# Optimization experiments

Hardware: AMD Instinct MI355X
Metric: run time of the kernel (lower is better)

## Reference

```python
import jax, jax.numpy as jnp
import numpy as np

LORA_ALPHA = 32
RANK = 16
TOP_K = 2
SCALING = LORA_ALPHA / RANK  # lora_alpha / r
EPS = 1e-9


def setup_inputs() -> dict:
    key = jax.random.key(0)
    ks = jax.random.split(key, 6)
    B, S, D_IN, D_OUT, E, R = 4, 2048, 4096, 4096, 8, RANK
    x = jax.random.normal(ks[0], (B, S, D_IN), dtype=jnp.float32)
    W = jax.random.normal(ks[1], (D_OUT, D_IN), dtype=jnp.float32) * (1.0 / np.sqrt(D_IN))
    bias = jax.random.normal(ks[2], (D_OUT,), dtype=jnp.float32) * 0.02
    route_W = jax.random.normal(ks[3], (E, D_IN), dtype=jnp.float32) * (1.0 / np.sqrt(D_IN))
    lora_A = jax.random.normal(ks[4], (E, R, D_IN), dtype=jnp.float32) * (1.0 / np.sqrt(D_IN))
    lora_B = jax.random.normal(ks[5], (D_OUT, R), dtype=jnp.float32)
    lora_B = jnp.broadcast_to(lora_B, (E, D_OUT, R)) * 0.01  # small nonzero so lora path matters
    return {"x": x, "W": W, "bias": bias, "route_W": route_W,
            "lora_A": lora_A, "lora_B": jnp.asarray(lora_B)}


def reference(x, W, bias, route_W, lora_A, lora_B):
    # Base dense projection: y = x W^T + b   [B,S,out]
    base = jnp.einsum('bsi,oi->bso', x, W) + bias

    # Router: softmax over experts in fp32, then top-k gating
    gate_score = jnp.einsum('bsi,ei->bse', x, route_W)          # [B,S,E]
    probs = jax.nn.softmax(gate_score.astype(jnp.float32), axis=-1)
    topk_vals, topk_idx = jax.lax.top_k(probs, TOP_K)           # [B,S,k]
    # renorm (top_k < lora_nums)
    topk_vals = topk_vals / (jnp.sum(topk_vals, axis=-1, keepdims=True) + EPS)
    # dense routing weights: zeros with top-k values scattered back  [B,S,E]
    E = probs.shape[-1]
    routing_weight = jnp.sum(
        jax.nn.one_hot(topk_idx, E, dtype=base.dtype) * topk_vals[..., None].astype(base.dtype),
        axis=-2)

    # Expert LoRA: identical math to the gather/index_add loop, expressed as
    # a dense weighted combine (weights are exactly 0 for unrouted experts).
    xf = x.astype(jnp.float32)
    h = jnp.einsum('bsi,eri->bser', xf, lora_A.astype(jnp.float32))      # [B,S,E,r] (small)
    hw = h * routing_weight.astype(jnp.float32)[..., None]               # gate per expert
    lora_out = jnp.einsum('bser,eor->bso', hw, lora_B.astype(jnp.float32))

    result = base + lora_out.astype(base.dtype) * SCALING
    return result, routing_weight, gate_score
```

## Files before the change

kernel.cpp:

```cpp
#include <hip/hip_runtime.h>
#include <hip/hip_bf16.h>

typedef __bf16 bf16_t;
typedef __bf16 bf16x8 __attribute__((ext_vector_type(8)));
typedef float floatx4 __attribute__((ext_vector_type(4)));

#define M_TOK 8192
#define K_DIM 4096
#define N_OUT 4096
#define NEXP  8
#define LRANK 16
#define KEXT  128
#define SCALING 2.0f

#define GLOAD_LDS16(g, l) \
    __builtin_amdgcn_global_load_lds((const __attribute__((address_space(1))) void*)(g), \
                                     (__attribute__((address_space(3))) void*)(l), 16, 0, 0)


__device__ __forceinline__ void pack4(bf16_t* dst, float4 v) {
    union { bf16_t h[4]; uint2 u; } t;
    t.h[0] = (bf16_t)v.x; t.h[1] = (bf16_t)v.y;
    t.h[2] = (bf16_t)v.z; t.h[3] = (bf16_t)v.w;
    *(uint2*)dst = t.u;
}

__device__ __forceinline__ void cvt8_body(const float* __restrict__ src,
                                          bf16_t* __restrict__ dst, int blk) {
    size_t i = (size_t)blk * 256 + threadIdx.x;
    float4 a = ((const float4*)src)[i * 2];
    float4 b = ((const float4*)src)[i * 2 + 1];
    union { bf16_t h[8]; uint4 u; } t;
    t.h[0] = (bf16_t)a.x; t.h[1] = (bf16_t)a.y; t.h[2] = (bf16_t)a.z; t.h[3] = (bf16_t)a.w;
    t.h[4] = (bf16_t)b.x; t.h[5] = (bf16_t)b.y; t.h[6] = (bf16_t)b.z; t.h[7] = (bf16_t)b.w;
    ((uint4*)dst)[i] = t.u;
}


#define GATE_BLKS     (M_TOK / 16)
#define PREP_W_BLKS   8192
#define PREP_A_BLKS   256
#define PREP_B_BLKS   2048

__global__ __launch_bounds__(256) void prep_gate(const float* __restrict__ x,
                                                 const float* __restrict__ routeW,
                                                 const float* __restrict__ W,
                                                 const float* __restrict__ loraA,
                                                 const float* __restrict__ loraB,
                                                 bf16_t* __restrict__ xb,
                                                 bf16_t* __restrict__ Wb,
                                                 bf16_t* __restrict__ aflat,
                                                 bf16_t* __restrict__ bflat,
                                                 float* __restrict__ rw_out,
                                                 float* __restrict__ gate_out)
{
    __shared__ float rwT[NEXP][256];

    if (blockIdx.x >= GATE_BLKS) {
        int b = blockIdx.x - GATE_BLKS;
        if (b < PREP_W_BLKS) {
            cvt8_body(W, Wb, b);
        } else if (b < PREP_W_BLKS + PREP_A_BLKS) {
            cvt8_body(loraA, aflat, b - PREP_W_BLKS);
        } else {
            int g = (b - PREP_W_BLKS - PREP_A_BLKS) * 256 + threadIdx.x;
            int o = g >> 7, j = g & 127;
            int e = j >> 4, r = j & 15;
            bflat[g] = (bf16_t)loraB[((size_t)e * N_OUT + o) * LRANK + r];
        }
        return;
    }

    int tid = threadIdx.x, lane = tid & 63, wave = tid >> 6;
    int tl = lane >> 4, seg = lane & 15;
    int t = blockIdx.x * 16 + wave * 4 + tl;
    const float* xrow = x + (size_t)t * K_DIM;
    bf16_t* xbrow = xb + (size_t)t * K_DIM;

    float acc[NEXP];
    #pragma unroll
    for (int e = 0; e < NEXP; ++e) acc[e] = 0.f;

    int srow = tid >> 5, scol = (tid & 31) * 8;

    for (int kk = 0; kk < K_DIM / 256; ++kk) {
        {
            const float4* src = (const float4*)(routeW + (size_t)srow * K_DIM + kk * 256 + scol);
            float4 v0 = src[0], v1 = src[1];
            *(float4*)&rwT[srow][scol]     = v0;
            *(float4*)&rwT[srow][scol + 4] = v1;
        }
        __syncthreads();
        #pragma unroll
        for (int kc = 0; kc < 4; ++kc) {
            int kloc = kc * 64 + seg * 4;
            int k = kk * 256 + kloc;
            float4 xv = *(const float4*)(xrow + k);
            union { bf16_t h[4]; uint2 u; } cv;
            cv.h[0] = (bf16_t)xv.x; cv.h[1] = (bf16_t)xv.y;
            cv.h[2] = (bf16_t)xv.z; cv.h[3] = (bf16_t)xv.w;
            *(uint2*)(xbrow + k) = cv.u;
            #pragma unroll
            for (int e = 0; e < NEXP; ++e) {
                float4 wv = *(const float4*)&rwT[e][kloc];
                acc[e] += xv.x * wv.x + xv.y * wv.y + xv.z * wv.z + xv.w * wv.w;
            }
        }
        __syncthreads();
    }

    #pragma unroll
    for (int e = 0; e < NEXP; ++e) {
        acc[e] += __shfl_xor(acc[e], 1);
        acc[e] += __shfl_xor(acc[e], 2);
        acc[e] += __shfl_xor(acc[e], 4);
        acc[e] += __shfl_xor(acc[e], 8);
    }

    if (seg == 0) {
        float mx = acc[0];
        #pragma unroll
        for (int e = 1; e < NEXP; ++e) mx = fmaxf(mx, acc[e]);
        float p[NEXP], s = 0.f;
        #pragma unroll
        for (int e = 0; e < NEXP; ++e) { p[e] = expf(acc[e] - mx); s += p[e]; }
        float inv_s = 1.0f / s;
        #pragma unroll
        for (int e = 0; e < NEXP; ++e) p[e] *= inv_s;
        int i0 = 0;
        #pragma unroll
        for (int e = 1; e < NEXP; ++e) if (p[e] > p[i0]) i0 = e;
        int i1 = (i0 == 0) ? 1 : 0;
        #pragma unroll
        for (int e = 0; e < NEXP; ++e) { if (e == i0 || e == i1) continue; if (p[e] > p[i1]) i1 = e; }
        float v0 = p[i0], v1 = p[i1];
        float inv = 1.0f / (v0 + v1 + 1e-9f);
        float r[NEXP];
        #pragma unroll
        for (int e = 0; e < NEXP; ++e) r[e] = 0.f;
        r[i0] = v0 * inv; r[i1] = v1 * inv;
        #pragma unroll
        for (int e = 0; e < NEXP; ++e) {
            gate_out[(size_t)t * NEXP + e] = acc[e];
            rw_out[(size_t)t * NEXP + e]  = r[e];
        }
    }
}


__global__ __launch_bounds__(256) void h_kernel_v3(const bf16_t* __restrict__ xb,
                                                   const bf16_t* __restrict__ aflat,
                                                   const float* __restrict__ rw,
                                                   bf16_t* __restrict__ hw)
{
    __shared__ bf16_t As[4 * 32 * 32];
    __shared__ bf16_t Bs[4 * 128 * 32];
    int tid = threadIdx.x, lane = tid & 63, wave = tid >> 6;
    int lrow = lane & 15, lq = lane >> 4;
    int n0 = wave * 32;
    int m0 = blockIdx.x * 32;
    floatx4 acc[2][2] = {};

    const bf16_t* srcA[2];
    #pragma unroll
    for (int i = 0; i < 2; ++i) {
        int idx = i * 256 + tid;
        int ks = idx >> 7, r = (idx >> 2) & 31, cc2 = idx & 3;
        srcA[i] = xb + (size_t)(m0 + r) * K_DIM + ks * 32 + cc2 * 8;
    }
    const bf16_t* srcB[8];
    #pragma unroll
    for (int i = 0; i < 8; ++i) {
        int idx = i * 256 + tid;
        int ks = idx >> 9, r = (idx >> 2) & 127, cc2 = idx & 3;
        srcB[i] = aflat + (size_t)r * K_DIM + ks * 32 + cc2 * 8;
    }

    for (int k0 = 0; k0 < K_DIM; k0 += 128) {
        #pragma unroll
        for (int i = 0; i < 2; ++i)
            GLOAD_LDS16(srcA[i] + k0, (char*)As + (i * 256 + wave * 64) * 16);
        #pragma unroll
        for (int i = 0; i < 8; ++i)
            GLOAD_LDS16(srcB[i] + k0, (char*)Bs + (i * 256 + wave * 64) * 16);
        __syncthreads();
        #pragma unroll
        for (int ks = 0; ks < 4; ++ks) {
            bf16x8 af[2], bfr[2];
            #pragma unroll
            for (int mi = 0; mi < 2; ++mi)
                af[mi] = *(const bf16x8*)(As + ks * 1024 + (mi * 16 + lrow) * 32 + lq * 8);
            #pragma unroll
            for (int ni = 0; ni < 2; ++ni)
                bfr[ni] = *(const bf16x8*)(Bs + ks * 4096 + (n0 + ni * 16 + lrow) * 32 + lq * 8);
            #pragma unroll
            for (int mi = 0; mi < 2; ++mi)
                #pragma unroll
                for (int ni = 0; ni < 2; ++ni)
                    acc[mi][ni] = __builtin_amdgcn_mfma_f32_16x16x32_bf16(af[mi], bfr[ni], acc[mi][ni], 0, 0, 0);
        }
        __syncthreads();
    }
    #pragma unroll
    for (int mi = 0; mi < 2; ++mi)
        #pragma unroll
        for (int ni = 0; ni < 2; ++ni)
            #pragma unroll
            for (int reg = 0; reg < 4; ++reg) {
                int t = m0 + mi * 16 + lq * 4 + reg;
                int j = n0 + ni * 16 + lrow;
                float g = rw[(size_t)t * NEXP + (j >> 4)] * SCALING;
                hw[(size_t)t * KEXT + j] = (bf16_t)(acc[mi][ni][reg] * g);
            }
}


#define BM 256
#define BN 256
#define BK 64
#define NT ((K_DIM + KEXT) / BK)

#define STAGE_A(ttv, nxtv, jv) do {                                                         \
    const bf16_t* g_ = ((ttv) < K_DIM / BK)                                                 \
        ? xb + oA + (size_t)(ttv) * BK + (size_t)(jv) * (64 * K_DIM)                        \
        : hw + oEA + (size_t)((ttv) - K_DIM / BK) * BK + (size_t)(jv) * (64 * KEXT);        \
    GLOAD_LDS16(g_, ldA + (nxtv) * (BM * BK * 2) + (jv) * 8192); } while (0)

#define STAGE_B(ttv, nxtv, jv) do {                                                         \
    const bf16_t* g_ = ((ttv) < K_DIM / BK)                                                 \
        ? Wb + oB + (size_t)(ttv) * BK + (size_t)(jv) * (64 * K_DIM)                        \
        : bflat + oEB + (size_t)((ttv) - K_DIM / BK) * BK + (size_t)(jv) * (64 * KEXT);     \
    GLOAD_LDS16(g_, ldB + (nxtv) * (BN * BK * 2) + (jv) * 8192); } while (0)

__global__ __launch_bounds__(512) void main_gemm_v5(const bf16_t* __restrict__ xb,
                                                    const bf16_t* __restrict__ Wb,
                                                    const float* __restrict__ bias,
                                                    const bf16_t* __restrict__ hw,
                                                    const bf16_t* __restrict__ bflat,
                                                    float* __restrict__ out)
{
    __shared__ __align__(16) bf16_t As[2][BM * BK];
    __shared__ __align__(16) bf16_t Bs[2][BN * BK];
    int tid = threadIdx.x, lane = tid & 63, wave = tid >> 6;
    int lrow = lane & 15, lq = lane >> 4;
    int wm = (wave >> 2) * 128;
    int wn = (wave & 3) * 64;

    int lin = blockIdx.y * gridDim.x + blockIdx.x;
    int swzb = (lin & 7) * 64 + (lin >> 3);
    int tm = (swzb >> 4) * BM;
    int tn = (swzb & 15) * BN;

    int swz = lrow & 7;
    int go0 = (lq ^ swz) * 8;
    int go1 = ((4 + lq) ^ swz) * 8;

    int rb = tid >> 3;
    int lg8 = ((tid & 7) ^ (rb & 7)) * 8;
    size_t oA  = (size_t)(tm + rb) * K_DIM + lg8;
    size_t oB  = (size_t)(tn + rb) * K_DIM + lg8;
    size_t oEA = (size_t)(tm + rb) * KEXT + lg8;
    size_t oEB = (size_t)(tn + rb) * KEXT + lg8;
    char* ldA = (char*)As + wave * 1024;
    char* ldB = (char*)Bs + wave * 1024;

    floatx4 acc[8][4] = {};

    #pragma unroll
    for (int j = 0; j < 4; ++j) {
        STAGE_A(0, 0, j);
        STAGE_B(0, 0, j);
    }
    asm volatile("s_waitcnt vmcnt(0)" ::: "memory");
    __builtin_amdgcn_sched_barrier(0);
    __builtin_amdgcn_s_barrier();

    for (int t = 0; t < NT; ++t) {
        int cur = t & 1, nxt = cur ^ 1;
        const bf16_t* curA = &As[cur][(wm + lrow) * BK];
        const bf16_t* curB = &Bs[cur][(wn + lrow) * BK];
        bool pf = (t + 1 < NT);
        int tt = t + 1;

        bf16x8 afA[4][2], afB[4][2], bf0[2][2], bf1[2][2];

        #pragma unroll
        for (int f = 0; f < 4; ++f) {
            afA[f][0] = *(const bf16x8*)(curA + (f * 16) * BK + go0);
            afA[f][1] = *(const bf16x8*)(curA + (f * 16) * BK + go1);
        }
        #pragma unroll
        for (int n = 0; n < 2; ++n) {
            bf0[n][0] = *(const bf16x8*)(curB + (n * 16) * BK + go0);
            bf0[n][1] = *(const bf16x8*)(curB + (n * 16) * BK + go1);
        }
        if (pf) { STAGE_B(tt, nxt, 0); STAGE_B(tt, nxt, 1); }
        __builtin_amdgcn_s_barrier();
        asm volatile("s_waitcnt lgkmcnt(0)" ::: "memory");
        __builtin_amdgcn_sched_barrier(0);
        __builtin_amdgcn_s_setprio(1);
        #pragma unroll
        for (int f = 0; f < 4; ++f)
            #pragma unroll
            for (int n = 0; n < 2; ++n)
                #pragma unroll
                for (int ks = 0; ks < 2; ++ks)
                    acc[f][n] = __builtin_amdgcn_mfma_f32_16x16x32_bf16(afA[f][ks], bf0[n][ks], acc[f][n], 0, 0, 0);
        __builtin_amdgcn_s_setprio(0);
        __builtin_amdgcn_s_barrier();

        #pragma unroll
        for (int n = 0; n < 2; ++n) {
            bf1[n][0] = *(const bf16x8*)(curB + (32 + n * 16) * BK + go0);
            bf1[n][1] = *(const bf16x8*)(curB + (32 + n * 16) * BK + go1);
        }
        if (pf) { STAGE_B(tt, nxt, 2); STAGE_B(tt, nxt, 3); }
        __builtin_amdgcn_s_barrier();
        asm volatile("s_waitcnt lgkmcnt(0)" ::: "memory");
        __builtin_amdgcn_sched_barrier(0);
        __builtin_amdgcn_s_setprio(1);
        #pragma unroll
        for (int f = 0; f < 4; ++f)
            #pragma unroll
            for (int n = 0; n < 2; ++n)
                #pragma unroll
                for (int ks = 0; ks < 2; ++ks)
                    acc[f][2 + n] = __builtin_amdgcn_mfma_f32_16x16x32_bf16(afA[f][ks], bf1[n][ks], acc[f][2 + n], 0, 0, 0);
        __builtin_amdgcn_s_setprio(0);
        if (pf) { asm volatile("s_waitcnt vmcnt(4)" ::: "memory"); }
        else    { asm volatile("s_waitcnt vmcnt(0)" ::: "memory"); }
        __builtin_amdgcn_sched_barrier(0);
        __builtin_amdgcn_s_barrier();

        #pragma unroll
        for (int f = 0; f < 4; ++f) {
            afB[f][0] = *(const bf16x8*)(curA + (64 + f * 16) * BK + go0);
            afB[f][1] = *(const bf16x8*)(curA + (64 + f * 16) * BK + go1);
        }
        if (pf) { STAGE_A(tt, nxt, 0); STAGE_A(tt, nxt, 2); }
        __builtin_amdgcn_s_barrier();
        asm volatile("s_waitcnt lgkmcnt(0)" ::: "memory");
        __builtin_amdgcn_sched_barrier(0);
        __builtin_amdgcn_s_setprio(1);
        #pragma unroll
        for (int f = 0; f < 4; ++f)
            #pragma unroll
            for (int n = 0; n < 2; ++n)
                #pragma unroll
                for (int ks = 0; ks < 2; ++ks)
                    acc[4 + f][n] = __builtin_amdgcn_mfma_f32_16x16x32_bf16(afB[f][ks], bf0[n][ks], acc[4 + f][n], 0, 0, 0);
        __builtin_amdgcn_s_setprio(0);
        __builtin_amdgcn_s_barrier();

        if (pf) { STAGE_A(tt, nxt, 1); STAGE_A(tt, nxt, 3); }
        __builtin_amdgcn_s_barrier();
        __builtin_amdgcn_s_setprio(1);
        #pragma unroll
        for (int f = 0; f < 4; ++f)
            #pragma unroll
            for (int n = 0; n < 2; ++n)
                #pragma unroll
                for (int ks = 0; ks < 2; ++ks)
                    acc[4 + f][2 + n] = __builtin_amdgcn_mfma_f32_16x16x32_bf16(afB[f][ks], bf1[n][ks], acc[4 + f][2 + n], 0, 0, 0);
        __builtin_amdgcn_s_setprio(0);
        if (pf) {
            asm volatile("s_waitcnt vmcnt(2)" ::: "memory");
            __builtin_amdgcn_sched_barrier(0);
        }
        __builtin_amdgcn_s_barrier();
    }

    #pragma unroll
    for (int mh = 0; mh < 2; ++mh)
        #pragma unroll
        for (int f = 0; f < 4; ++f)
            #pragma unroll
            for (int nh = 0; nh < 2; ++nh)
                #pragma unroll
                for (int n = 0; n < 2; ++n) {
                    int row = tm + wm + mh * 64 + f * 16 + lq * 4;
                    int col = tn + wn + nh * 32 + n * 16 + lrow;
                    float b = bias[col];
                    #pragma unroll
                    for (int reg = 0; reg < 4; ++reg)
                        out[(size_t)(row + reg) * N_OUT + col] = acc[mh * 4 + f][nh * 2 + n][reg] + b;
                }
}


__global__ __launch_bounds__(256) void prep_bflat(const float* __restrict__ loraB,
                                                  bf16_t* __restrict__ bflat) {
    int g = blockIdx.x * 256 + threadIdx.x;
    int o = g >> 7, j = g & 127;
    int e = j >> 4, r = j & 15;
    bflat[g] = (bf16_t)loraB[((size_t)e * N_OUT + o) * LRANK + r];
}

__global__ __launch_bounds__(256) void gate_kernel(const float* __restrict__ x,
                                                   const float* __restrict__ routeW,
                                                   float* __restrict__ rw_out,
                                                   float* __restrict__ gate_out)
{
    int wave = threadIdx.x >> 6;
    int lane = threadIdx.x & 63;
    int t = blockIdx.x * 4 + wave;
    const float4* xp = (const float4*)(x + (size_t)t * K_DIM);
    float acc[NEXP];
    #pragma unroll
    for (int e = 0; e < NEXP; ++e) acc[e] = 0.f;
    #pragma unroll 4
    for (int it = 0; it < K_DIM / 256; ++it) {
        float4 xv = xp[it * 64 + lane];
        #pragma unroll
        for (int e = 0; e < NEXP; ++e) {
            float4 wv = ((const float4*)(routeW + (size_t)e * K_DIM))[it * 64 + lane];
            acc[e] += xv.x * wv.x + xv.y * wv.y + xv.z * wv.z + xv.w * wv.w;
        }
    }
    #pragma unroll
    for (int e = 0; e < NEXP; ++e)
        for (int off = 32; off > 0; off >>= 1)
            acc[e] += __shfl_xor(acc[e], off, 64);
    if (lane == 0) {
        float mx = acc[0];
        #pragma unroll
        for (int e = 1; e < NEXP; ++e) mx = fmaxf(mx, acc[e]);
        float p[NEXP], s = 0.f;
        #pragma unroll
        for (int e = 0; e < NEXP; ++e) { p[e] = expf(acc[e] - mx); s += p[e]; }
        float inv_s = 1.0f / s;
        #pragma unroll
        for (int e = 0; e < NEXP; ++e) p[e] *= inv_s;
        int i0 = 0;
        #pragma unroll
        for (int e = 1; e < NEXP; ++e) if (p[e] > p[i0]) i0 = e;
        int i1 = (i0 == 0) ? 1 : 0;
        #pragma unroll
        for (int e = 0; e < NEXP; ++e) { if (e == i0 || e == i1) continue; if (p[e] > p[i1]) i1 = e; }
        float v0 = p[i0], v1 = p[i1];
        float inv = 1.0f / (v0 + v1 + 1e-9f);
        float r[NEXP];
        #pragma unroll
        for (int e = 0; e < NEXP; ++e) r[e] = 0.f;
        r[i0] = v0 * inv; r[i1] = v1 * inv;
        #pragma unroll
        for (int e = 0; e < NEXP; ++e) {
            gate_out[(size_t)t * NEXP + e] = acc[e];
            rw_out[(size_t)t * NEXP + e]  = r[e];
        }
    }
}

__global__ __launch_bounds__(256) void h_kernel(const float* __restrict__ x,
                                                const float* __restrict__ loraA,
                                                const float* __restrict__ rw,
                                                bf16_t* __restrict__ hw)
{
    __shared__ bf16_t As[32][40];
    __shared__ bf16_t Bs[128][40];
    int tid = threadIdx.x;
    int wave = tid >> 6, lane = tid & 63;
    int lrow = lane & 15, lq = lane >> 4;
    int m0 = blockIdx.x * 32;
    floatx4 acc[2][2] = {};
    int rb = tid >> 1, cb = (tid & 1) * 16;
    for (int k0 = 0; k0 < K_DIM; k0 += 32) {
        if (tid < 64) {
            const float* srcA = x + (size_t)(m0 + rb) * K_DIM + k0 + cb;
            #pragma unroll
            for (int q = 0; q < 4; ++q) pack4(&As[rb][cb + q * 4], ((const float4*)srcA)[q]);
        }
        {
            const float* srcB = loraA + (size_t)rb * K_DIM + k0 + cb;
            #pragma unroll
            for (int q = 0; q < 4; ++q) pack4(&Bs[rb][cb + q * 4], ((const float4*)srcB)[q]);
        }
        __syncthreads();
        bf16x8 af[2], bfr[2];
        #pragma unroll
        for (int mi = 0; mi < 2; ++mi) af[mi] = *(const bf16x8*)&As[mi * 16 + lrow][lq * 8];
        #pragma unroll
        for (int ni = 0; ni < 2; ++ni) bfr[ni] = *(const bf16x8*)&Bs[wave * 32 + ni * 16 + lrow][lq * 8];
        #pragma unroll
        for (int mi = 0; mi < 2; ++mi)
            #pragma unroll
            for (int ni = 0; ni < 2; ++ni)
                acc[mi][ni] = __builtin_amdgcn_mfma_f32_16x16x32_bf16(af[mi], bfr[ni], acc[mi][ni], 0, 0, 0);
        __syncthreads();
    }
    #pragma unroll
    for (int mi = 0; mi < 2; ++mi)
        #pragma unroll
        for (int ni = 0; ni < 2; ++ni)
            #pragma unroll
            for (int reg = 0; reg < 4; ++reg) {
                int t = m0 + mi * 16 + lq * 4 + reg;
                int j = wave * 32 + ni * 16 + lrow;
                float g = rw[(size_t)t * NEXP + (j >> 4)] * SCALING;
                hw[(size_t)t * KEXT + j] = (bf16_t)(acc[mi][ni][reg] * g);
            }
}

__device__ __forceinline__ void mma_step(const bf16_t (*As)[40], const bf16_t (*Bs)[40],
                                         floatx4 acc[4][4], int wm, int wn, int lrow, int lq) {
    bf16x8 af[4], bfr[4];
    #pragma unroll
    for (int mi = 0; mi < 4; ++mi) af[mi] = *(const bf16x8*)&As[wm + mi * 16 + lrow][lq * 8];
    #pragma unroll
    for (int ni = 0; ni < 4; ++ni) bfr[ni] = *(const bf16x8*)&Bs[wn + ni * 16 + lrow][lq * 8];
    #pragma unroll
    for (int mi = 0; mi < 4; ++mi)
        #pragma unroll
        for (int ni = 0; ni < 4; ++ni)
            acc[mi][ni] = __builtin_amdgcn_mfma_f32_16x16x32_bf16(af[mi], bfr[ni], acc[mi][ni], 0, 0, 0);
}

__global__ __launch_bounds__(256) void main_gemm(const float* __restrict__ x,
                                                 const float* __restrict__ W,
                                                 const float* __restrict__ bias,
                                                 const bf16_t* __restrict__ hw,
                                                 const bf16_t* __restrict__ bflat,
                                                 float* __restrict__ out)
{
    __shared__ bf16_t As[128][40];
    __shared__ bf16_t Bs[128][40];
    int tid = threadIdx.x, lane = tid & 63, wave = tid >> 6;
    int lrow = lane & 15, lq = lane >> 4;
    int wm = (wave >> 1) * 64, wn = (wave & 1) * 64;
    int tm = blockIdx.y * 128, tn = blockIdx.x * 128;
    floatx4 acc[4][4] = {};
    int rb = tid >> 1, cb = (tid & 1) * 16;
    const float* gA = x + (size_t)(tm + rb) * K_DIM + cb;
    const float* gB = W + (size_t)(tn + rb) * K_DIM + cb;
    for (int k0 = 0; k0 < K_DIM; k0 += 32) {
        #pragma unroll
        for (int q = 0; q < 4; ++q) {
            pack4(&As[rb][cb + q * 4], ((const float4*)(gA + k0))[q]);
            pack4(&Bs[rb][cb + q * 4], ((const float4*)(gB + k0))[q]);
        }
        __syncthreads();
        mma_step(As, Bs, acc, wm, wn, lrow, lq);
        __syncthreads();
    }
    const bf16_t* eA = hw    + (size_t)(tm + rb) * KEXT + cb;
    const bf16_t* eB = bflat + (size_t)(tn + rb) * KEXT + cb;
    for (int k0 = 0; k0 < KEXT; k0 += 32) {
        *(uint4*)&As[rb][cb]     = *(const uint4*)(eA + k0);
        *(uint4*)&As[rb][cb + 8] = *(const uint4*)(eA + k0 + 8);
        *(uint4*)&Bs[rb][cb]     = *(const uint4*)(eB + k0);
        *(uint4*)&Bs[rb][cb + 8] = *(const uint4*)(eB + k0 + 8);
        __syncthreads();
        mma_step(As, Bs, acc, wm, wn, lrow, lq);
        __syncthreads();
    }
    #pragma unroll
    for (int mi = 0; mi < 4; ++mi)
        #pragma unroll
        for (int ni = 0; ni < 4; ++ni) {
            int row = tm + wm + mi * 16 + lq * 4;
            int col = tn + wn + ni * 16 + lrow;
            float b = bias[col];
            #pragma unroll
            for (int reg = 0; reg < 4; ++reg)
                out[(size_t)(row + reg) * N_OUT + col] = acc[mi][ni][reg] + b;
        }
}


extern "C" void kernel_launch(void* const* d_in, const int* in_sizes, int n_in,
                              void* d_out, int out_size, void* d_ws, size_t ws_size,
                              hipStream_t stream) {
    const float* x      = (const float*)d_in[0];
    const float* W      = (const float*)d_in[1];
    const float* bias   = (const float*)d_in[2];
    const float* routeW = (const float*)d_in[3];
    const float* loraA  = (const float*)d_in[4];
    const float* loraB  = (const float*)d_in[5];

    float* out0 = (float*)d_out;
    float* out1 = out0 + (size_t)M_TOK * N_OUT;
    float* out2 = out1 + (size_t)M_TOK * NEXP;

    size_t need = ((size_t)M_TOK * K_DIM + (size_t)N_OUT * K_DIM +
                   (size_t)KEXT * K_DIM + (size_t)N_OUT * KEXT +
                   (size_t)M_TOK * KEXT) * sizeof(bf16_t);

    if (ws_size >= need) {
        bf16_t* xb    = (bf16_t*)d_ws;
        bf16_t* Wb    = xb + (size_t)M_TOK * K_DIM;
        bf16_t* aflat = Wb + (size_t)N_OUT * K_DIM;
        bf16_t* bflat = aflat + (size_t)KEXT * K_DIM;
        bf16_t* hw    = bflat + (size_t)N_OUT * KEXT;

        hipLaunchKernelGGL(prep_gate, dim3(GATE_BLKS + PREP_W_BLKS + PREP_A_BLKS + PREP_B_BLKS),
                           dim3(256), 0, stream,
                           x, routeW, W, loraA, loraB, xb, Wb, aflat, bflat, out1, out2);
        hipLaunchKernelGGL(h_kernel_v3, dim3(M_TOK / 32), dim3(256), 0, stream, xb, aflat, out1, hw);
        hipLaunchKernelGGL(main_gemm_v5, dim3(N_OUT / 256, M_TOK / 256), dim3(512), 0, stream,
                           xb, Wb, bias, hw, bflat, out0);
    } else {
        bf16_t* bflat = (bf16_t*)d_ws;
        bf16_t* hw    = bflat + (size_t)N_OUT * KEXT;
        hipLaunchKernelGGL(prep_bflat, dim3((N_OUT * KEXT) / 256), dim3(256), 0, stream, loraB, bflat);
        hipLaunchKernelGGL(gate_kernel, dim3(M_TOK / 4), dim3(256), 0, stream, x, routeW, out1, out2);
        hipLaunchKernelGGL(h_kernel, dim3(M_TOK / 32), dim3(256), 0, stream, x, loraA, out1, hw);
        hipLaunchKernelGGL(main_gemm, dim3(N_OUT / 128, M_TOK / 128), dim3(256), 0, stream,
                           x, W, bias, hw, bflat, out0);
    }
}
```

Before: 577.7 us.

## Prefetch GEMM tiles two iterations ahead with half-tile LDS staging

Restructures the main GEMM's global-to-LDS pipeline. Each iteration now issues the loads for tile t+2 into the same double buffer it is currently consuming, and only does so once the relevant halves have been read into registers. The prologue fills both stages up front, and the vmcnt waits are adjusted so one iteration's worth of loads stays in flight across a whole compute phase. This aims to hide more memory latency without extra LDS. The cost is that loads are issued later within each iteration, and the barrier ordering becomes more delicate.

```diff
diff --git a/kernel.cpp b/kernel.cpp
--- a/kernel.cpp
+++ b/kernel.cpp
@@ -220,31 +220,28 @@
 #define BK 64
 #define NT ((K_DIM + KEXT) / BK)
 
-#define STAGE_A(ttv, nxtv, jv) do {                                                         \
-    const bf16_t* g_ = ((ttv) < K_DIM / BK)                                                 \
-        ? xb + oA + (size_t)(ttv) * BK + (size_t)(jv) * (64 * K_DIM)                        \
-        : hw + oEA + (size_t)((ttv) - K_DIM / BK) * BK + (size_t)(jv) * (64 * KEXT);        \
-    GLOAD_LDS16(g_, ldA + (nxtv) * (BM * BK * 2) + (jv) * 8192); } while (0)
-
-#define STAGE_B(ttv, nxtv, jv) do {                                                         \
-    const bf16_t* g_ = ((ttv) < K_DIM / BK)                                                 \
-        ? Wb + oB + (size_t)(ttv) * BK + (size_t)(jv) * (64 * K_DIM)                        \
-        : bflat + oEB + (size_t)((ttv) - K_DIM / BK) * BK + (size_t)(jv) * (64 * KEXT);     \
-    GLOAD_LDS16(g_, ldB + (nxtv) * (BN * BK * 2) + (jv) * 8192); } while (0)
-
-__global__ __launch_bounds__(512) void main_gemm_v5(const bf16_t* __restrict__ xb,
+#define STAGE_HALF(opb, gbulk, gext, ob, oe, ttv, u, jv) do {                                \
+    const bf16_t* g_ = ((ttv) < K_DIM / BK)                                                  \
+        ? gbulk + ob + (size_t)((u) * 128 + (jv) * 64) * K_DIM + (size_t)(ttv) * BK          \
+        : gext  + oe + (size_t)((u) * 128 + (jv) * 64) * KEXT                                \
+                     + (size_t)((ttv) - K_DIM / BK) * BK;                                    \
+    GLOAD_LDS16(g_, (char*)opb + ((ttv) & 1) * 32768 + (u) * 16384 + (jv) * 8192 + wave * 1024); } while (0)
+
+__global__ __launch_bounds__(512) void main_gemm_v6(const bf16_t* __restrict__ xb,
                                                     const bf16_t* __restrict__ Wb,
                                                     const float* __restrict__ bias,
                                                     const bf16_t* __restrict__ hw,
                                                     const bf16_t* __restrict__ bflat,
                                                     float* __restrict__ out)
 {
-    __shared__ __align__(16) bf16_t As[2][BM * BK];
-    __shared__ __align__(16) bf16_t Bs[2][BN * BK];
+    __shared__ __align__(16) bf16_t As[2][2][128 * BK];
+    __shared__ __align__(16) bf16_t Bs[2][2][128 * BK];
     int tid = threadIdx.x, lane = tid & 63, wave = tid >> 6;
     int lrow = lane & 15, lq = lane >> 4;
-    int wm = (wave >> 2) * 128;
+    int ha = wave >> 2;
     int wn = (wave & 3) * 64;
+    int hb = wn >> 7;
+    int wnr = wn & 64;
 
     int lin = blockIdx.y * gridDim.x + blockIdx.x;
     int swzb = (lin & 7) * 64 + (lin >> 3);
@@ -261,26 +258,33 @@
     size_t oB  = (size_t)(tn + rb) * K_DIM + lg8;
     size_t oEA = (size_t)(tm + rb) * KEXT + lg8;
     size_t oEB = (size_t)(tn + rb) * KEXT + lg8;
-    char* ldA = (char*)As + wave * 1024;
-    char* ldB = (char*)Bs + wave * 1024;
 
     floatx4 acc[8][4] = {};
 
     #pragma unroll
-    for (int j = 0; j < 4; ++j) {
-        STAGE_A(0, 0, j);
-        STAGE_B(0, 0, j);
-    }
-    asm volatile("s_waitcnt vmcnt(0)" ::: "memory");
+    for (int u = 0; u < 2; ++u)
+        #pragma unroll
+        for (int j = 0; j < 2; ++j) {
+            STAGE_HALF(As, xb, hw, oA, oEA, 0, u, j);
+            STAGE_HALF(Bs, Wb, bflat, oB, oEB, 0, u, j);
+        }
+    #pragma unroll
+    for (int u = 0; u < 2; ++u)
+        #pragma unroll
+        for (int j = 0; j < 2; ++j) {
+            STAGE_HALF(As, xb, hw, oA, oEA, 1, u, j);
+            STAGE_HALF(Bs, Wb, bflat, oB, oEB, 1, u, j);
+        }
+    asm volatile("s_waitcnt vmcnt(8)" ::: "memory");
     __builtin_amdgcn_sched_barrier(0);
     __builtin_amdgcn_s_barrier();
 
     for (int t = 0; t < NT; ++t) {
-        int cur = t & 1, nxt = cur ^ 1;
-        const bf16_t* curA = &As[cur][(wm + lrow) * BK];
-        const bf16_t* curB = &Bs[cur][(wn + lrow) * BK];
-        bool pf = (t + 1 < NT);
-        int tt = t + 1;
+        int cur = t & 1;
+        const bf16_t* curA = (const bf16_t*)((const char*)As + cur * 32768 + ha * 16384) + lrow * BK;
+        const bf16_t* curB = (const bf16_t*)((const char*)Bs + cur * 32768 + hb * 16384) + (wnr + lrow) * BK;
+        bool pf2 = (t + 2 < NT);
+        int tt2 = t + 2;
 
         bf16x8 afA[4][2], afB[4][2], bf0[2][2], bf1[2][2];
 
@@ -294,7 +298,6 @@
             bf0[n][0] = *(const bf16x8*)(curB + (n * 16) * BK + go0);
             bf0[n][1] = *(const bf16x8*)(curB + (n * 16) * BK + go1);
         }
-        if (pf) { STAGE_B(tt, nxt, 0); STAGE_B(tt, nxt, 1); }
         __builtin_amdgcn_s_barrier();
         asm volatile("s_waitcnt lgkmcnt(0)" ::: "memory");
         __builtin_amdgcn_sched_barrier(0);
@@ -314,7 +317,6 @@
             bf1[n][0] = *(const bf16x8*)(curB + (32 + n * 16) * BK + go0);
             bf1[n][1] = *(const bf16x8*)(curB + (32 + n * 16) * BK + go1);
         }
-        if (pf) { STAGE_B(tt, nxt, 2); STAGE_B(tt, nxt, 3); }
         __builtin_amdgcn_s_barrier();
         asm volatile("s_waitcnt lgkmcnt(0)" ::: "memory");
         __builtin_amdgcn_sched_barrier(0);
@@ -327,9 +329,6 @@
                 for (int ks = 0; ks < 2; ++ks)
                     acc[f][2 + n] = __builtin_amdgcn_mfma_f32_16x16x32_bf16(afA[f][ks], bf1[n][ks], acc[f][2 + n], 0, 0, 0);
         __builtin_amdgcn_s_setprio(0);
-        if (pf) { asm volatile("s_waitcnt vmcnt(4)" ::: "memory"); }
-        else    { asm volatile("s_waitcnt vmcnt(0)" ::: "memory"); }
-        __builtin_amdgcn_sched_barrier(0);
         __builtin_amdgcn_s_barrier();
 
         #pragma unroll
@@ -337,7 +336,7 @@
             afB[f][0] = *(const bf16x8*)(curA + (64 + f * 16) * BK + go0);
             afB[f][1] = *(const bf16x8*)(curA + (64 + f * 16) * BK + go1);
         }
-        if (pf) { STAGE_A(tt, nxt, 0); STAGE_A(tt, nxt, 2); }
+        if (pf2) { STAGE_HALF(Bs, Wb, bflat, oB, oEB, tt2, 0, 0); STAGE_HALF(Bs, Wb, bflat, oB, oEB, tt2, 0, 1); }
         __builtin_amdgcn_s_barrier();
         asm volatile("s_waitcnt lgkmcnt(0)" ::: "memory");
         __builtin_amdgcn_sched_barrier(0);
@@ -352,7 +351,11 @@
         __builtin_amdgcn_s_setprio(0);
         __builtin_amdgcn_s_barrier();
 
-        if (pf) { STAGE_A(tt, nxt, 1); STAGE_A(tt, nxt, 3); }
+        if (pf2) {
+            STAGE_HALF(Bs, Wb, bflat, oB, oEB, tt2, 1, 0); STAGE_HALF(Bs, Wb, bflat, oB, oEB, tt2, 1, 1);
+            STAGE_HALF(As, xb, hw, oA, oEA, tt2, 0, 0);    STAGE_HALF(As, xb, hw, oA, oEA, tt2, 0, 1);
+            STAGE_HALF(As, xb, hw, oA, oEA, tt2, 1, 0);    STAGE_HALF(As, xb, hw, oA, oEA, tt2, 1, 1);
+        }
         __builtin_amdgcn_s_barrier();
         __builtin_amdgcn_s_setprio(1);
         #pragma unroll
@@ -363,8 +366,11 @@
                 for (int ks = 0; ks < 2; ++ks)
                     acc[4 + f][2 + n] = __builtin_amdgcn_mfma_f32_16x16x32_bf16(afB[f][ks], bf1[n][ks], acc[4 + f][2 + n], 0, 0, 0);
         __builtin_amdgcn_s_setprio(0);
-        if (pf) {
-            asm volatile("s_waitcnt vmcnt(2)" ::: "memory");
+        if (pf2) {
+            asm volatile("s_waitcnt vmcnt(8)" ::: "memory");
+            __builtin_amdgcn_sched_barrier(0);
+        } else if (t + 1 < NT) {
+            asm volatile("s_waitcnt vmcnt(0)" ::: "memory");
             __builtin_amdgcn_sched_barrier(0);
         }
         __builtin_amdgcn_s_barrier();
@@ -378,7 +384,7 @@
             for (int nh = 0; nh < 2; ++nh)
                 #pragma unroll
                 for (int n = 0; n < 2; ++n) {
-                    int row = tm + wm + mh * 64 + f * 16 + lq * 4;
+                    int row = tm + ha * 128 + mh * 64 + f * 16 + lq * 4;
                     int col = tn + wn + nh * 32 + n * 16 + lrow;
                     float b = bias[col];
                     #pragma unroll
@@ -596,7 +602,7 @@
                            dim3(256), 0, stream,
                            x, routeW, W, loraA, loraB, xb, Wb, aflat, bflat, out1, out2);
         hipLaunchKernelGGL(h_kernel_v3, dim3(M_TOK / 32), dim3(256), 0, stream, xb, aflat, out1, hw);
-        hipLaunchKernelGGL(main_gemm_v5, dim3(N_OUT / 256, M_TOK / 256), dim3(512), 0, stream,
+        hipLaunchKernelGGL(main_gemm_v6, dim3(N_OUT / 256, M_TOK / 256), dim3(512), 0, stream,
                            xb, Wb, bias, hw, bflat, out0);
     } else {
         bf16_t* bflat = (bf16_t*)d_ws;
```

Measured after the change: 604.4 us. 4.6% more time.
